# Kernel tuning notes

Hardware: AMD Instinct MI355X
Metric: run time of the kernel (lower is better)

Reference implementation:

```python
import jax, jax.numpy as jnp
import numpy as np

T, D, H = 2048, 2048, 16
C = D // H  # head dim = 128

def setup_inputs() -> dict:
    key = jax.random.key(0)
    k1, k2, k3 = jax.random.split(key, 3)
    x = jax.random.normal(k1, (T, D), dtype=jnp.float32)
    W_attn = jax.random.normal(k2, (3 * D, D), dtype=jnp.float32) * 0.02
    W_proj = jax.random.normal(k3, (D, D), dtype=jnp.float32) * 0.02
    return {"x": x, "W_attn": W_attn, "W_proj": W_proj}

def reference(x, W_attn, W_proj):
    # c_attn: per-token Linear -> [T, 3D]
    qkv = x @ W_attn.T
    q, k, v = jnp.split(qkv, 3, axis=-1)  # each [T, D]
    # [T, D] -> [H, T, C]
    q = q.reshape(T, H, C).transpose(1, 0, 2)
    k = k.reshape(T, H, C).transpose(1, 0, 2)
    v = v.reshape(T, H, C).transpose(1, 0, 2)
    # raw scores [H, T, T]
    scores = jnp.einsum('htc,hsc->hts', q, k)
    causal_mask = jnp.tril(jnp.ones((1, T, T))) == 0
    scores = jnp.where(causal_mask, float('-inf'), scores)
    orig_dtype = scores.dtype
    # NOTE: original scales AFTER masking, inside softmax, in fp32
    attn = jax.nn.softmax(scores.astype(jnp.float32) / jnp.sqrt(jnp.float32(C)), axis=-1)
    attn = attn.astype(orig_dtype)
    out = attn @ v  # [H, T, C]
    out = out.transpose(1, 0, 2).reshape(T, D)
    return out @ W_proj.T
```

## Files before the change

### kernel.cpp

```cpp
#include <hip/hip_runtime.h>
#include <hip/hip_bf16.h>
#include <stdint.h>

typedef __attribute__((ext_vector_type(8))) __bf16 bf16x8;
typedef __attribute__((ext_vector_type(4))) float f32x4;
typedef __attribute__((ext_vector_type(4))) unsigned int u32x4;
typedef __attribute__((ext_vector_type(4))) unsigned short u16x4;

__device__ __forceinline__ unsigned short f2bf(float f) {
  union { float f; unsigned int u; } v; v.f = f;
  unsigned int r = v.u + 0x7fffu + ((v.u >> 16) & 1u);
  return (unsigned short)(r >> 16);
}

__device__ __forceinline__ void gload_lds16(const void* g, void* l) {
  __builtin_amdgcn_global_load_lds(
      (const __attribute__((address_space(1))) unsigned int*)g,
      (__attribute__((address_space(3))) unsigned int*)l, 16, 0, 0);
}

__global__ __launch_bounds__(256) void cast_f32_bf16(const float* __restrict__ in,
                                                     unsigned short* __restrict__ out,
                                                     int n) {
  int i = (blockIdx.x * 256 + threadIdx.x) * 4;
  if (i >= n) return;
  f32x4 v = *(const f32x4*)&in[i];
  u16x4 o;
  o[0] = f2bf(v[0]); o[1] = f2bf(v[1]); o[2] = f2bf(v[2]); o[3] = f2bf(v[3]);
  *(u16x4*)&out[i] = o;
}

template<int OUT_BF16>
__global__ __launch_bounds__(256) void gemm_bt(const unsigned short* __restrict__ A,
                                               const unsigned short* __restrict__ B,
                                               void* __restrict__ Cv,
                                               int M, int N, int K) {
  __shared__ unsigned short As[2][128 * 32];
  __shared__ unsigned short Bs[2][128 * 32];

  const int tid  = threadIdx.x;
  const int lane = tid & 63;
  const int wave = tid >> 6;
  const int wr = (wave >> 1) * 64;
  const int wc = (wave & 1) * 64;
  const int row0 = blockIdx.y * 128;
  const int col0 = blockIdx.x * 128;
  const int l16 = lane & 15;
  const int lk  = (lane >> 4) * 8;

  const int srow = lane >> 2;
  const int sc   = (lane & 3) * 8;

  f32x4 acc[4][4] = {};

#pragma unroll
  for (int i = 0; i < 2; ++i) {
    int t = wave * 2 + i;
    int r = t * 16 + srow;
    gload_lds16(&A[(size_t)(row0 + r) * K + sc], &As[0][t * 512]);
    gload_lds16(&B[(size_t)(col0 + r) * K + sc], &Bs[0][t * 512]);
  }
  __syncthreads();

  int cur = 0;
  for (int k0 = 0; k0 < K; k0 += 32, cur ^= 1) {
    if (k0 + 32 < K) {
#pragma unroll
      for (int i = 0; i < 2; ++i) {
        int t = wave * 2 + i;
        int r = t * 16 + srow;
        gload_lds16(&A[(size_t)(row0 + r) * K + k0 + 32 + sc], &As[cur ^ 1][t * 512]);
        gload_lds16(&B[(size_t)(col0 + r) * K + k0 + 32 + sc], &Bs[cur ^ 1][t * 512]);
      }
    }

    bf16x8 af[4], bfr[4];
#pragma unroll
    for (int i = 0; i < 4; ++i) af[i]  = *(const bf16x8*)&As[cur][(wr + i * 16 + l16) * 32 + lk];
#pragma unroll
    for (int i = 0; i < 4; ++i) bfr[i] = *(const bf16x8*)&Bs[cur][(wc + i * 16 + l16) * 32 + lk];
#pragma unroll
    for (int i = 0; i < 4; ++i)
#pragma unroll
      for (int j = 0; j < 4; ++j)
        acc[i][j] = __builtin_amdgcn_mfma_f32_16x16x32_bf16(af[i], bfr[j], acc[i][j], 0, 0, 0);

    __syncthreads();
  }

  const int orow = (lane >> 4) * 4;
#pragma unroll
  for (int i = 0; i < 4; ++i)
#pragma unroll
    for (int j = 0; j < 4; ++j)
#pragma unroll
      for (int r = 0; r < 4; ++r) {
        size_t gr = row0 + wr + i * 16 + orow + r;
        size_t gc = col0 + wc + j * 16 + l16;
        float v = acc[i][j][r];
        if (OUT_BF16) ((unsigned short*)Cv)[gr * N + gc] = f2bf(v);
        else          ((float*)Cv)[gr * N + gc] = v;
      }
}

#define KS_IDX(r, c) ((((r) * 128) + (c)) ^ (((r) & 7) << 3))
#define VT_IDX(c, t) ((((c) * 64)  + (t)) ^ (((c) & 7) << 3))
#define PS_IDX(q, c) ((((q) * 64)  + (c)) ^ (((q) & 7) << 3))

__global__ __launch_bounds__(256, 2) void attn_kernel(const unsigned short* __restrict__ qkv,
                                                      unsigned short* __restrict__ ctx) {
  __shared__ unsigned short Ks[64 * 128];
  __shared__ unsigned short VTs[128 * 64];
  __shared__ unsigned short Ps[4][16 * 64];

  const int tid  = threadIdx.x;
  const int lane = tid & 63;
  const int w    = tid >> 6;
  const int l16  = lane & 15;
  const int lk8  = (lane >> 4) * 8;

  const int flat = blockIdx.x + blockIdx.y * 32;
  int h, qb;
  if (flat < 256) { h = flat >> 5; qb = flat & 31; }
  else            { int f2 = flat - 256; h = 8 + (f2 >> 5); qb = 31 - (f2 & 31); }

  const int qrow = qb * 64 + w * 16;

  bf16x8 qf[4];
#pragma unroll
  for (int kk = 0; kk < 4; ++kk)
    qf[kk] = *(const bf16x8*)&qkv[(size_t)(qrow + l16) * 6144 + h * 128 + kk * 32 + lk8];

  f32x4 o[8] = {};
  float m[4], lsum[4];
#pragma unroll
  for (int r = 0; r < 4; ++r) { m[r] = -1e30f; lsum[r] = 0.f; }

  const float sscale = 0.08838834764831845f * 1.4426950408889634f;
  const int qg0 = qrow + (lane >> 4) * 4;

  const int t0v = (tid & 15) * 4;
  const int c0v = (tid >> 4) * 8;

  const int nkb = qb + 1;
  for (int kb = 0; kb < nkb; ++kb) {
    u32x4 kreg[4], vreg[4];
#pragma unroll
    for (int it = 0; it < 4; ++it) {
      int idx = it * 256 + tid;
      int row = idx >> 4, c0 = (idx & 15) * 8;
      kreg[it] = *(const u32x4*)&qkv[(size_t)(kb * 64 + row) * 6144 + 2048 + h * 128 + c0];
    }
#pragma unroll
    for (int r = 0; r < 4; ++r)
      vreg[r] = *(const u32x4*)&qkv[(size_t)(kb * 64 + t0v + r) * 6144 + 4096 + h * 128 + c0v];

    __syncthreads();

#pragma unroll
    for (int it = 0; it < 4; ++it) {
      int idx = it * 256 + tid;
      int row = idx >> 4, c0 = (idx & 15) * 8;
      *(u32x4*)&Ks[KS_IDX(row, c0)] = kreg[it];
    }
    {
      const unsigned short* p0 = (const unsigned short*)&vreg[0];
      const unsigned short* p1 = (const unsigned short*)&vreg[1];
      const unsigned short* p2 = (const unsigned short*)&vreg[2];
      const unsigned short* p3 = (const unsigned short*)&vreg[3];
#pragma unroll
      for (int j = 0; j < 8; ++j) {
        u16x4 wv; wv[0] = p0[j]; wv[1] = p1[j]; wv[2] = p2[j]; wv[3] = p3[j];
        *(u16x4*)&VTs[VT_IDX(c0v + j, t0v)] = wv;
      }
    }
    __syncthreads();

    f32x4 s[4] = {};
#pragma unroll
    for (int kk = 0; kk < 4; ++kk)
#pragma unroll
      for (int n = 0; n < 4; ++n) {
        bf16x8 kf = *(const bf16x8*)&Ks[KS_IDX(n * 16 + l16, kk * 32 + lk8)];
        s[n] = __builtin_amdgcn_mfma_f32_16x16x32_bf16(qf[kk], kf, s[n], 0, 0, 0);
      }

    const bool diag = (kb == qb);
    float rmax[4];
#pragma unroll
    for (int r = 0; r < 4; ++r) rmax[r] = -1e30f;
#pragma unroll
    for (int n = 0; n < 4; ++n) {
      int kg = kb * 64 + n * 16 + l16;
#pragma unroll
      for (int r = 0; r < 4; ++r) {
        float v = s[n][r] * sscale;
        if (diag && kg > qg0 + r) v = -1e30f;
        s[n][r] = v;
        rmax[r] = fmaxf(rmax[r], v);
      }
    }
#pragma unroll
    for (int d = 1; d < 16; d <<= 1)
#pragma unroll
      for (int r = 0; r < 4; ++r) rmax[r] = fmaxf(rmax[r], __shfl_xor(rmax[r], d));

    float alpha[4];
#pragma unroll
    for (int r = 0; r < 4; ++r) {
      float mn = fmaxf(m[r], rmax[r]);
      alpha[r] = exp2f(m[r] - mn);
      m[r] = mn;
    }
    float rsum[4] = {0.f, 0.f, 0.f, 0.f};
#pragma unroll
    for (int n = 0; n < 4; ++n)
#pragma unroll
      for (int r = 0; r < 4; ++r) {
        float p = exp2f(s[n][r] - m[r]);
        s[n][r] = p;
        rsum[r] += p;
      }
#pragma unroll
    for (int d = 1; d < 16; d <<= 1)
#pragma unroll
      for (int r = 0; r < 4; ++r) rsum[r] += __shfl_xor(rsum[r], d);
#pragma unroll
    for (int r = 0; r < 4; ++r) lsum[r] = lsum[r] * alpha[r] + rsum[r];

#pragma unroll
    for (int n = 0; n < 8; ++n)
#pragma unroll
      for (int r = 0; r < 4; ++r) o[n][r] *= alpha[r];

#pragma unroll
    for (int n = 0; n < 4; ++n)
#pragma unroll
      for (int r = 0; r < 4; ++r)
        Ps[w][PS_IDX((lane >> 4) * 4 + r, n * 16 + l16)] = f2bf(s[n][r]);
    asm volatile("s_waitcnt lgkmcnt(0)" ::: "memory");

#pragma unroll
    for (int kk = 0; kk < 2; ++kk) {
      bf16x8 pf = *(const bf16x8*)&Ps[w][PS_IDX(l16, kk * 32 + lk8)];
#pragma unroll
      for (int n = 0; n < 8; ++n) {
        bf16x8 vf = *(const bf16x8*)&VTs[VT_IDX(n * 16 + l16, kk * 32 + lk8)];
        o[n] = __builtin_amdgcn_mfma_f32_16x16x32_bf16(pf, vf, o[n], 0, 0, 0);
      }
    }
  }

#pragma unroll
  for (int r = 0; r < 4; ++r) {
    float inv = 1.0f / lsum[r];
    size_t gr = qrow + (lane >> 4) * 4 + r;
#pragma unroll
    for (int n = 0; n < 8; ++n)
      ctx[gr * 2048 + h * 128 + n * 16 + l16] = f2bf(o[n][r] * inv);
  }
}

extern "C" void kernel_launch(void* const* d_in, const int* in_sizes, int n_in,
                              void* d_out, int out_size, void* d_ws, size_t ws_size,
                              hipStream_t stream) {
  const float* x  = (const float*)d_in[0];
  const float* Wa = (const float*)d_in[1];
  const float* Wp = (const float*)d_in[2];
  float* out = (float*)d_out;

  char* ws = (char*)d_ws;
  unsigned short* xb   = (unsigned short*)(ws);
  unsigned short* wab  = (unsigned short*)(ws + 8388608);
  unsigned short* wpb  = (unsigned short*)(ws + 33554432);
  unsigned short* qkvb = (unsigned short*)(ws + 41943040);
  unsigned short* ctx  = (unsigned short*)(ws + 67108864);

  cast_f32_bf16<<<4096, 256, 0, stream>>>(x, xb, 2048 * 2048);
  cast_f32_bf16<<<12288, 256, 0, stream>>>(Wa, wab, 6144 * 2048);
  cast_f32_bf16<<<4096, 256, 0, stream>>>(Wp, wpb, 2048 * 2048);

  gemm_bt<1><<<dim3(48, 16), 256, 0, stream>>>(xb, wab, qkvb, 2048, 6144, 2048);

  attn_kernel<<<dim3(32, 16), 256, 0, stream>>>(qkvb, ctx);

  gemm_bt<0><<<dim3(16, 16), 256, 0, stream>>>(ctx, wpb, out, 2048, 2048, 2048);
}
```

Baseline: 301.0 us.

## Split-K output projection, direct-global K loads, double-buffered V, lazy softmax rescale

The output projection GEMM becomes split-K over two z-slices, writing a partial fp32 buffer that a new add kernel reduces, to get more blocks in flight when the workspace is large enough. The attention kernel drops K staging in LDS and reads K fragments directly from global memory. V is double-buffered in LDS with the next tile prefetched, which removes one barrier per iteration, and the launch bound occupancy hint rises to 4. The online softmax now rescales only when the running max grows by more than a threshold and defers the row-sum reduction to the end. The cost is an extra reduction pass with fp32 traffic and uncached global K reads.

```diff
diff --git a/kernel.cpp b/kernel.cpp
--- a/kernel.cpp
+++ b/kernel.cpp
@@ -30,11 +30,22 @@
   *(u16x4*)&out[i] = o;
 }
 
+__global__ __launch_bounds__(256) void addf32(float* __restrict__ out,
+                                              const float* __restrict__ part, int n) {
+  int i = (blockIdx.x * 256 + threadIdx.x) * 4;
+  if (i >= n) return;
+  f32x4 a = *(const f32x4*)&out[i];
+  f32x4 b = *(const f32x4*)&part[i];
+  a[0] += b[0]; a[1] += b[1]; a[2] += b[2]; a[3] += b[3];
+  *(f32x4*)&out[i] = a;
+}
+
 template<int OUT_BF16>
 __global__ __launch_bounds__(256) void gemm_bt(const unsigned short* __restrict__ A,
                                                const unsigned short* __restrict__ B,
                                                void* __restrict__ Cv,
-                                               int M, int N, int K) {
+                                               float* __restrict__ Cp,
+                                               int M, int N, int K, int KS) {
   __shared__ unsigned short As[2][128 * 32];
   __shared__ unsigned short Bs[2][128 * 32];
 
@@ -47,6 +58,7 @@
   const int col0 = blockIdx.x * 128;
   const int l16 = lane & 15;
   const int lk  = (lane >> 4) * 8;
+  const int kbeg = blockIdx.z * KS;
 
   const int srow = lane >> 2;
   const int sc   = (lane & 3) * 8;
@@ -57,14 +69,14 @@
   for (int i = 0; i < 2; ++i) {
     int t = wave * 2 + i;
     int r = t * 16 + srow;
-    gload_lds16(&A[(size_t)(row0 + r) * K + sc], &As[0][t * 512]);
-    gload_lds16(&B[(size_t)(col0 + r) * K + sc], &Bs[0][t * 512]);
+    gload_lds16(&A[(size_t)(row0 + r) * K + kbeg + sc], &As[0][t * 512]);
+    gload_lds16(&B[(size_t)(col0 + r) * K + kbeg + sc], &Bs[0][t * 512]);
   }
   __syncthreads();
 
   int cur = 0;
-  for (int k0 = 0; k0 < K; k0 += 32, cur ^= 1) {
-    if (k0 + 32 < K) {
+  for (int k0 = kbeg; k0 < kbeg + KS; k0 += 32, cur ^= 1) {
+    if (k0 + 32 < kbeg + KS) {
 #pragma unroll
       for (int i = 0; i < 2; ++i) {
         int t = wave * 2 + i;
@@ -88,6 +100,8 @@
     __syncthreads();
   }
 
+  void* outp = (blockIdx.z == 0) ? Cv : (void*)Cp;
+
   const int orow = (lane >> 4) * 4;
 #pragma unroll
   for (int i = 0; i < 4; ++i)
@@ -98,19 +112,17 @@
         size_t gr = row0 + wr + i * 16 + orow + r;
         size_t gc = col0 + wc + j * 16 + l16;
         float v = acc[i][j][r];
-        if (OUT_BF16) ((unsigned short*)Cv)[gr * N + gc] = f2bf(v);
-        else          ((float*)Cv)[gr * N + gc] = v;
-      }
-}
-
-#define KS_IDX(r, c) ((((r) * 128) + (c)) ^ (((r) & 7) << 3))
-#define VT_IDX(c, t) ((((c) * 64)  + (t)) ^ (((c) & 7) << 3))
-#define PS_IDX(q, c) ((((q) * 64)  + (c)) ^ (((q) & 7) << 3))
-
-__global__ __launch_bounds__(256, 2) void attn_kernel(const unsigned short* __restrict__ qkv,
+        if (OUT_BF16) ((unsigned short*)outp)[gr * N + gc] = f2bf(v);
+        else          ((float*)outp)[gr * N + gc] = v;
+      }
+}
+
+#define VT_IDX(c, t) ((((c) * 64) + (t)) ^ (((((c) ^ ((c) >> 3))) & 7) << 3))
+#define PS_IDX(q, c) ((((q) * 64) + (c)) ^ (((q) & 7) << 3))
+
+__global__ __launch_bounds__(256, 4) void attn_kernel(const unsigned short* __restrict__ qkv,
                                                       unsigned short* __restrict__ ctx) {
-  __shared__ unsigned short Ks[64 * 128];
-  __shared__ unsigned short VTs[128 * 64];
+  __shared__ unsigned short VTs[2][128 * 64];
   __shared__ unsigned short Ps[4][16 * 64];
 
   const int tid  = threadIdx.x;
@@ -126,15 +138,18 @@
 
   const int qrow = qb * 64 + w * 16;
 
+  const unsigned short* Kbase = qkv + 2048 + h * 128;
+  const unsigned short* Vbase = qkv + 4096 + h * 128;
+
   bf16x8 qf[4];
 #pragma unroll
   for (int kk = 0; kk < 4; ++kk)
     qf[kk] = *(const bf16x8*)&qkv[(size_t)(qrow + l16) * 6144 + h * 128 + kk * 32 + lk8];
 
   f32x4 o[8] = {};
-  float m[4], lsum[4];
-#pragma unroll
-  for (int r = 0; r < 4; ++r) { m[r] = -1e30f; lsum[r] = 0.f; }
+  float m[4], ls[4];
+#pragma unroll
+  for (int r = 0; r < 4; ++r) { m[r] = -1e30f; ls[r] = 0.f; }
 
   const float sscale = 0.08838834764831845f * 1.4426950408889634f;
   const int qg0 = qrow + (lane >> 4) * 4;
@@ -142,53 +157,63 @@
   const int t0v = (tid & 15) * 4;
   const int c0v = (tid >> 4) * 8;
 
+  {
+    u32x4 vr[4];
+#pragma unroll
+    for (int r = 0; r < 4; ++r)
+      vr[r] = *(const u32x4*)&Vbase[(size_t)(t0v + r) * 6144 + c0v];
+    const unsigned short* p0 = (const unsigned short*)&vr[0];
+    const unsigned short* p1 = (const unsigned short*)&vr[1];
+    const unsigned short* p2 = (const unsigned short*)&vr[2];
+    const unsigned short* p3 = (const unsigned short*)&vr[3];
+#pragma unroll
+    for (int j = 0; j < 8; ++j) {
+      u16x4 wv; wv[0] = p0[j]; wv[1] = p1[j]; wv[2] = p2[j]; wv[3] = p3[j];
+      *(u16x4*)&VTs[0][VT_IDX(c0v + j, t0v)] = wv;
+    }
+  }
+
   const int nkb = qb + 1;
   for (int kb = 0; kb < nkb; ++kb) {
-    u32x4 kreg[4], vreg[4];
-#pragma unroll
-    for (int it = 0; it < 4; ++it) {
-      int idx = it * 256 + tid;
-      int row = idx >> 4, c0 = (idx & 15) * 8;
-      kreg[it] = *(const u32x4*)&qkv[(size_t)(kb * 64 + row) * 6144 + 2048 + h * 128 + c0];
-    }
-#pragma unroll
-    for (int r = 0; r < 4; ++r)
-      vreg[r] = *(const u32x4*)&qkv[(size_t)(kb * 64 + t0v + r) * 6144 + 4096 + h * 128 + c0v];
+    const int cur = kb & 1;
+    const bool pre = (kb + 1 < nkb);
+
+    u32x4 vr[4];
+    if (pre) {
+#pragma unroll
+      for (int r = 0; r < 4; ++r)
+        vr[r] = *(const u32x4*)&Vbase[(size_t)((kb + 1) * 64 + t0v + r) * 6144 + c0v];
+    }
 
     __syncthreads();
 
-#pragma unroll
-    for (int it = 0; it < 4; ++it) {
-      int idx = it * 256 + tid;
-      int row = idx >> 4, c0 = (idx & 15) * 8;
-      *(u32x4*)&Ks[KS_IDX(row, c0)] = kreg[it];
-    }
-    {
-      const unsigned short* p0 = (const unsigned short*)&vreg[0];
-      const unsigned short* p1 = (const unsigned short*)&vreg[1];
-      const unsigned short* p2 = (const unsigned short*)&vreg[2];
-      const unsigned short* p3 = (const unsigned short*)&vreg[3];
+    if (pre) {
+      const unsigned short* p0 = (const unsigned short*)&vr[0];
+      const unsigned short* p1 = (const unsigned short*)&vr[1];
+      const unsigned short* p2 = (const unsigned short*)&vr[2];
+      const unsigned short* p3 = (const unsigned short*)&vr[3];
 #pragma unroll
       for (int j = 0; j < 8; ++j) {
         u16x4 wv; wv[0] = p0[j]; wv[1] = p1[j]; wv[2] = p2[j]; wv[3] = p3[j];
-        *(u16x4*)&VTs[VT_IDX(c0v + j, t0v)] = wv;
-      }
-    }
-    __syncthreads();
+        *(u16x4*)&VTs[cur ^ 1][VT_IDX(c0v + j, t0v)] = wv;
+      }
+    }
 
     f32x4 s[4] = {};
 #pragma unroll
-    for (int kk = 0; kk < 4; ++kk)
-#pragma unroll
-      for (int n = 0; n < 4; ++n) {
-        bf16x8 kf = *(const bf16x8*)&Ks[KS_IDX(n * 16 + l16, kk * 32 + lk8)];
+    for (int n = 0; n < 4; ++n) {
+      const unsigned short* krow = &Kbase[(size_t)(kb * 64 + n * 16 + l16) * 6144];
+#pragma unroll
+      for (int kk = 0; kk < 4; ++kk) {
+        bf16x8 kf = *(const bf16x8*)&krow[kk * 32 + lk8];
         s[n] = __builtin_amdgcn_mfma_f32_16x16x32_bf16(qf[kk], kf, s[n], 0, 0, 0);
       }
+    }
 
     const bool diag = (kb == qb);
-    float rmax[4];
-#pragma unroll
-    for (int r = 0; r < 4; ++r) rmax[r] = -1e30f;
+    float pmax[4];
+#pragma unroll
+    for (int r = 0; r < 4; ++r) pmax[r] = -1e30f;
 #pragma unroll
     for (int n = 0; n < 4; ++n) {
       int kg = kb * 64 + n * 16 + l16;
@@ -197,47 +222,36 @@
         float v = s[n][r] * sscale;
         if (diag && kg > qg0 + r) v = -1e30f;
         s[n][r] = v;
-        rmax[r] = fmaxf(rmax[r], v);
-      }
-    }
-#pragma unroll
-    for (int d = 1; d < 16; d <<= 1)
-#pragma unroll
-      for (int r = 0; r < 4; ++r) rmax[r] = fmaxf(rmax[r], __shfl_xor(rmax[r], d));
-
-    float alpha[4];
-#pragma unroll
-    for (int r = 0; r < 4; ++r) {
-      float mn = fmaxf(m[r], rmax[r]);
-      alpha[r] = exp2f(m[r] - mn);
-      m[r] = mn;
-    }
-    float rsum[4] = {0.f, 0.f, 0.f, 0.f};
+        pmax[r] = fmaxf(pmax[r], v);
+      }
+    }
+
+    bool need = (pmax[0] > m[0] + 8.f) | (pmax[1] > m[1] + 8.f) |
+                (pmax[2] > m[2] + 8.f) | (pmax[3] > m[3] + 8.f);
+    if (__ballot(need)) {
+#pragma unroll
+      for (int d = 1; d < 16; d <<= 1)
+#pragma unroll
+        for (int r = 0; r < 4; ++r) pmax[r] = fmaxf(pmax[r], __shfl_xor(pmax[r], d));
+#pragma unroll
+      for (int r = 0; r < 4; ++r) {
+        float mn = fmaxf(m[r], pmax[r]);
+        float alpha = exp2f(m[r] - mn);
+        m[r] = mn;
+        ls[r] *= alpha;
+#pragma unroll
+        for (int n = 0; n < 8; ++n) o[n][r] *= alpha;
+      }
+    }
+
 #pragma unroll
     for (int n = 0; n < 4; ++n)
 #pragma unroll
       for (int r = 0; r < 4; ++r) {
         float p = exp2f(s[n][r] - m[r]);
-        s[n][r] = p;
-        rsum[r] += p;
-      }
-#pragma unroll
-    for (int d = 1; d < 16; d <<= 1)
-#pragma unroll
-      for (int r = 0; r < 4; ++r) rsum[r] += __shfl_xor(rsum[r], d);
-#pragma unroll
-    for (int r = 0; r < 4; ++r) lsum[r] = lsum[r] * alpha[r] + rsum[r];
-
-#pragma unroll
-    for (int n = 0; n < 8; ++n)
-#pragma unroll
-      for (int r = 0; r < 4; ++r) o[n][r] *= alpha[r];
-
-#pragma unroll
-    for (int n = 0; n < 4; ++n)
-#pragma unroll
-      for (int r = 0; r < 4; ++r)
-        Ps[w][PS_IDX((lane >> 4) * 4 + r, n * 16 + l16)] = f2bf(s[n][r]);
+        ls[r] += p;
+        Ps[w][PS_IDX((lane >> 4) * 4 + r, n * 16 + l16)] = f2bf(p);
+      }
     asm volatile("s_waitcnt lgkmcnt(0)" ::: "memory");
 
 #pragma unroll
@@ -245,15 +259,20 @@
       bf16x8 pf = *(const bf16x8*)&Ps[w][PS_IDX(l16, kk * 32 + lk8)];
 #pragma unroll
       for (int n = 0; n < 8; ++n) {
-        bf16x8 vf = *(const bf16x8*)&VTs[VT_IDX(n * 16 + l16, kk * 32 + lk8)];
+        bf16x8 vf = *(const bf16x8*)&VTs[cur][VT_IDX(n * 16 + l16, kk * 32 + lk8)];
         o[n] = __builtin_amdgcn_mfma_f32_16x16x32_bf16(pf, vf, o[n], 0, 0, 0);
       }
     }
   }
 
 #pragma unroll
+  for (int d = 1; d < 16; d <<= 1)
+#pragma unroll
+    for (int r = 0; r < 4; ++r) ls[r] += __shfl_xor(ls[r], d);
+
+#pragma unroll
   for (int r = 0; r < 4; ++r) {
-    float inv = 1.0f / lsum[r];
+    float inv = 1.0f / ls[r];
     size_t gr = qrow + (lane >> 4) * 4 + r;
 #pragma unroll
     for (int n = 0; n < 8; ++n)
@@ -275,14 +294,24 @@
   unsigned short* wpb  = (unsigned short*)(ws + 33554432);
   unsigned short* qkvb = (unsigned short*)(ws + 41943040);
   unsigned short* ctx  = (unsigned short*)(ws + 67108864);
+  float* proj_part     = (float*)(ws + 75497472);
+  const bool splitk = ws_size >= (size_t)(75497472 + 16777216);
 
   cast_f32_bf16<<<4096, 256, 0, stream>>>(x, xb, 2048 * 2048);
   cast_f32_bf16<<<12288, 256, 0, stream>>>(Wa, wab, 6144 * 2048);
   cast_f32_bf16<<<4096, 256, 0, stream>>>(Wp, wpb, 2048 * 2048);
 
-  gemm_bt<1><<<dim3(48, 16), 256, 0, stream>>>(xb, wab, qkvb, 2048, 6144, 2048);
+  gemm_bt<1><<<dim3(48, 16, 1), 256, 0, stream>>>(xb, wab, qkvb, nullptr,
+                                                  2048, 6144, 2048, 2048);
 
   attn_kernel<<<dim3(32, 16), 256, 0, stream>>>(qkvb, ctx);
 
-  gemm_bt<0><<<dim3(16, 16), 256, 0, stream>>>(ctx, wpb, out, 2048, 2048, 2048);
-}
+  if (splitk) {
+    gemm_bt<0><<<dim3(16, 16, 2), 256, 0, stream>>>(ctx, wpb, out, proj_part,
+                                                    2048, 2048, 2048, 1024);
+    addf32<<<4096, 256, 0, stream>>>(out, proj_part, 2048 * 2048);
+  } else {
+    gemm_bt<0><<<dim3(16, 16, 1), 256, 0, stream>>>(ctx, wpb, out, nullptr,
+                                                    2048, 2048, 2048, 2048);
+  }
+}
```

After: 432.0 us. 43.5% more time.
